# Kernel tuning notes

Measured on AMD Instinct MI355X. Metric: run time of the kernel, lower is better.

The kernel has to match this reference:

```python
import jax, jax.numpy as jnp
import numpy as np

N_NODES = 50000

def _gcn_layer(x, src, dst, W, b, n_nodes):
    # x: [N, F_in]; src/dst: [E+N] (self-loops already appended)
    h = x @ W  # [N, F_out]
    deg = jax.ops.segment_sum(jnp.ones_like(dst, dtype=h.dtype), dst, num_segments=n_nodes)
    dinv = jnp.where(deg > 0, jax.lax.rsqrt(deg), 0.0)  # deg^{-1/2}
    norm = dinv[src] * dinv[dst]  # [E+N]
    msg = h[src] * norm[:, None]  # gather + scale
    out = jax.ops.segment_sum(msg, dst, num_segments=n_nodes)  # scatter-add
    return out + b

def setup_inputs() -> dict:
    key = jax.random.key(0)
    k1, k2, k3, k4 = jax.random.split(key, 4)
    d = 128
    E = 800000
    x = jax.random.normal(k1, (N_NODES, d), dtype=jnp.float32)
    edge_index = jax.random.randint(k2, (2, E), 0, N_NODES, dtype=jnp.int64)
    W1 = jax.random.normal(k3, (d, d), dtype=jnp.float32) / np.sqrt(d)
    b1 = jnp.zeros((d,), dtype=jnp.float32)
    W2 = jax.random.normal(k4, (d, d), dtype=jnp.float32) / np.sqrt(d)
    b2 = jnp.zeros((d,), dtype=jnp.float32)
    return {"x": x, "edge_index": edge_index, "W1": W1, "b1": b1, "W2": W2, "b2": b2}

def reference(x, edge_index, W1, b1, W2, b2):
    n = x.shape[0]
    loops = jnp.arange(n, dtype=edge_index.dtype)
    src = jnp.concatenate([edge_index[0], loops])  # add self-loops
    dst = jnp.concatenate([edge_index[1], loops])
    h = _gcn_layer(x, src, dst, W1, b1, n)
    h = jax.nn.relu(h)
    z = _gcn_layer(h, src, dst, W2, b2, n)
    return z
```

## Files before the change

### kernel.cpp

```cpp
#include <hip/hip_runtime.h>
#include <hip/hip_fp16.h>

#define NF 128
#define DMAX 64

typedef _Float16 half8  __attribute__((ext_vector_type(8)));
typedef _Float16 half4v __attribute__((ext_vector_type(4)));
typedef float    floatx4 __attribute__((ext_vector_type(4)));

__global__ __launch_bounds__(256) void z_k(
    int* __restrict__ cnt, int N, int zb,
    const float* __restrict__ W1, const float* __restrict__ W2,
    __half* __restrict__ WT1, __half* __restrict__ WT2)
{
    int b = blockIdx.x;
    if (b < zb) {
        int i = b * 256 + threadIdx.x;
        if (i <= N) cnt[i] = 0;
        return;
    }
    int idx = (b - zb) * 256 + threadIdx.x;
    const float* W = (idx < 16384) ? W1 : W2;
    __half* WT     = (idx < 16384) ? WT1 : WT2;
    int j = idx & 16383;
    int nn = j & 127, k = j >> 7;
    WT[nn * NF + k] = __float2half(W[k * NF + nn]);
}

__device__ __forceinline__ void fill_one(
    int d, int s, int* __restrict__ cnt, int* __restrict__ csrF,
    int* __restrict__ ovf, int N)
{
    int pos = atomicAdd(&cnt[d], 1);
    if (pos < DMAX) {
        csrF[(size_t)d * DMAX + pos] = s;
    } else {
        int o = atomicAdd(&cnt[N], 1);
        ovf[2 * o] = d; ovf[2 * o + 1] = s;
    }
}

__global__ __launch_bounds__(256) void fill_k(
    const int* __restrict__ src, const int* __restrict__ dst,
    int* __restrict__ cnt, int* __restrict__ csrF, int* __restrict__ ovf,
    int E, int N)
{
    int i4 = (blockIdx.x * 256 + threadIdx.x) * 4;
    if (i4 + 3 < E) {
        int4 d = *(const int4*)(dst + i4);
        int4 s = *(const int4*)(src + i4);
        fill_one(d.x, s.x, cnt, csrF, ovf, N);
        fill_one(d.y, s.y, cnt, csrF, ovf, N);
        fill_one(d.z, s.z, cnt, csrF, ovf, N);
        fill_one(d.w, s.w, cnt, csrF, ovf, N);
    } else {
        for (int e = i4; e < E; e++)
            fill_one(dst[e], src[e], cnt, csrF, ovf, N);
    }
}

__global__ __launch_bounds__(512) void gemm1_k(
    const float* __restrict__ X, const __half* __restrict__ WT,
    const int* __restrict__ cnt, __half* __restrict__ H, int M)
{
    __shared__ __half wlds[128][136];
    const int tid = threadIdx.x;
    {
        int r = tid >> 2;
        int c0 = (tid & 3) * 32;
        const half8* s = (const half8*)(WT + (size_t)r * NF + c0);
        half8* d = (half8*)&wlds[r][c0];
        #pragma unroll
        for (int j = 0; j < 4; j++) d[j] = s[j];
    }
    __syncthreads();

    const int wave = tid >> 6, lane = tid & 63;
    const int quad = lane >> 4, l15 = lane & 15;
    const int rowA = blockIdx.x * 128 + wave * 16 + l15;
    const int rowc = (rowA < M) ? rowA : (M - 1);

    half8 afr[4];
    #pragma unroll
    for (int kc = 0; kc < 4; kc++) {
        const floatx4* p = (const floatx4*)(X + (size_t)rowc * NF + kc * 32 + quad * 8);
        floatx4 u = p[0], v = p[1];
        half8 a;
        a[0] = (_Float16)u[0]; a[1] = (_Float16)u[1];
        a[2] = (_Float16)u[2]; a[3] = (_Float16)u[3];
        a[4] = (_Float16)v[0]; a[5] = (_Float16)v[1];
        a[6] = (_Float16)v[2]; a[7] = (_Float16)v[3];
        afr[kc] = a;
    }

    floatx4 acc[8];
    #pragma unroll
    for (int ct = 0; ct < 8; ct++) { floatx4 z = {0.f, 0.f, 0.f, 0.f}; acc[ct] = z; }

    #pragma unroll
    for (int kc = 0; kc < 4; kc++) {
        #pragma unroll
        for (int ct = 0; ct < 8; ct++) {
            half8 b = *(const half8*)&wlds[ct * 16 + l15][kc * 32 + quad * 8];
            acc[ct] = __builtin_amdgcn_mfma_f32_16x16x32_f16(afr[kc], b, acc[ct], 0, 0, 0);
        }
    }

    const int orow0 = blockIdx.x * 128 + wave * 16 + quad * 4;
    #pragma unroll
    for (int r = 0; r < 4; r++) {
        int orow = orow0 + r;
        if (orow < M) {
            float dv = rsqrtf((float)cnt[orow] + 1.0f);
            #pragma unroll
            for (int ct = 0; ct < 8; ct++)
                H[(size_t)orow * NF + ct * 16 + l15] = __float2half(acc[ct][r] * dv);
        }
    }
}

__device__ __forceinline__ void gather2w(
    const half8* __restrict__ hs8, const int* __restrict__ csrF,
    const int* __restrict__ cnt, int nA, int n,
    int g, int fl, int lane, floatx4& ac0, floatx4& ac1,
    const int* __restrict__ ovf, int novf)
{
    const int ep  = g & 1;
    const int isB = g >> 1;
    const int nB  = nA + 1;

    int cntA = (nA < n) ? cnt[nA] : 0;
    int cntB = (nB < n) ? cnt[nB] : 0;
    const int ccA = min(cntA, DMAX), ccB = min(cntB, DMAX);

    int idxA = (lane < ccA) ? __builtin_nontemporal_load(&csrF[(size_t)nA * DMAX + lane]) : 0;
    int idxB = (lane < ccB) ? __builtin_nontemporal_load(&csrF[(size_t)nB * DMAX + lane]) : 0;

    if (ep == 0) {
        int nd = isB ? nB : nA;
        if (nd < n) {
            half8 s = hs8[(size_t)nd * 16 + fl];
            ac0[0] += (float)s[0]; ac0[1] += (float)s[1];
            ac0[2] += (float)s[2]; ac0[3] += (float)s[3];
            ac1[0] += (float)s[4]; ac1[1] += (float)s[5];
            ac1[2] += (float)s[6]; ac1[3] += (float)s[7];
        }
    }

    const int myc  = isB ? ccB : ccA;
    const int maxc = max(ccA, ccB);
    for (int j = 0; j < maxc; j += 16) {
        int s[8];
        half8 v[8];
        #pragma unroll
        for (int t = 0; t < 8; t++) {
            int e = j + 2 * t + ep;
            int eA = min(e, ccA - 1); eA = (eA < 0) ? 0 : eA;
            int eB = min(e, ccB - 1); eB = (eB < 0) ? 0 : eB;
            int sa = __shfl(idxA, eA, 64);
            int sb = __shfl(idxB, eB, 64);
            s[t] = isB ? sb : sa;
        }
        #pragma unroll
        for (int t = 0; t < 8; t++)
            v[t] = hs8[(size_t)s[t] * 16 + fl];
        #pragma unroll
        for (int t = 0; t < 8; t++) {
            if (j + 2 * t + ep < myc) {
                ac0[0] += (float)v[t][0]; ac0[1] += (float)v[t][1];
                ac0[2] += (float)v[t][2]; ac0[3] += (float)v[t][3];
                ac1[0] += (float)v[t][4]; ac1[1] += (float)v[t][5];
                ac1[2] += (float)v[t][6]; ac1[3] += (float)v[t][7];
            }
        }
    }

    if (novf > 0 && ep == 0) {
        int myN = isB ? nB : nA;
        for (int i = 0; i < novf; i++) {
            int d = ovf[2 * i];
            if (d == myN) {
                half8 v = hs8[(size_t)ovf[2 * i + 1] * 16 + fl];
                ac0[0] += (float)v[0]; ac0[1] += (float)v[1];
                ac0[2] += (float)v[2]; ac0[3] += (float)v[3];
                ac1[0] += (float)v[4]; ac1[1] += (float)v[5];
                ac1[2] += (float)v[6]; ac1[3] += (float)v[7];
            }
        }
    }

    #pragma unroll
    for (int q = 0; q < 4; q++) {
        ac0[q] += __shfl_xor(ac0[q], 16, 64);
        ac1[q] += __shfl_xor(ac1[q], 16, 64);
    }
}

__global__ __launch_bounds__(512) void aggmm_k(
    const __half* __restrict__ hs, const int* __restrict__ csrF,
    const int* __restrict__ cnt, const float* __restrict__ bias,
    const __half* __restrict__ WT, __half* __restrict__ Hout, int n,
    const int* __restrict__ ovf)
{
    __shared__ __half alds[16][136];
    const int tid = threadIdx.x;
    const int wave = tid >> 6, lane = tid & 63;
    const int g = lane >> 4, fl = lane & 15;
    const int nb0 = blockIdx.x * 16;
    const int nA = nb0 + wave * 2;
    const int novf = cnt[n];

    floatx4 ac0 = {0.f, 0.f, 0.f, 0.f}, ac1 = {0.f, 0.f, 0.f, 0.f};
    gather2w((const half8*)hs, csrF, cnt, nA, n, g, fl, lane, ac0, ac1, ovf, novf);

    if ((g & 1) == 0) {
        int node = nA + (g >> 1);
        int row  = wave * 2 + (g >> 1);
        half8 hv;
        if (node < n) {
            float dv = rsqrtf((float)cnt[node] + 1.0f);
            const floatx4 bv0 = *(const floatx4*)&bias[fl * 8];
            const floatx4 bv1 = *(const floatx4*)&bias[fl * 8 + 4];
            hv[0] = (_Float16)fmaxf(dv * ac0[0] + bv0[0], 0.f);
            hv[1] = (_Float16)fmaxf(dv * ac0[1] + bv0[1], 0.f);
            hv[2] = (_Float16)fmaxf(dv * ac0[2] + bv0[2], 0.f);
            hv[3] = (_Float16)fmaxf(dv * ac0[3] + bv0[3], 0.f);
            hv[4] = (_Float16)fmaxf(dv * ac1[0] + bv1[0], 0.f);
            hv[5] = (_Float16)fmaxf(dv * ac1[1] + bv1[1], 0.f);
            hv[6] = (_Float16)fmaxf(dv * ac1[2] + bv1[2], 0.f);
            hv[7] = (_Float16)fmaxf(dv * ac1[3] + bv1[3], 0.f);
        } else {
            #pragma unroll
            for (int i = 0; i < 8; i++) hv[i] = (_Float16)0.f;
        }
        *(half8*)&alds[row][fl * 8] = hv;
    }
    __syncthreads();

    const int quad = lane >> 4, l15 = lane & 15;
    const int ct = wave;
    half8 afr[4];
    #pragma unroll
    for (int kc = 0; kc < 4; kc++)
        afr[kc] = *(const half8*)&alds[l15][kc * 32 + quad * 8];

    floatx4 o0 = {0.f, 0.f, 0.f, 0.f};
    #pragma unroll
    for (int kc = 0; kc < 4; kc++) {
        half8 b = *(const half8*)(WT + (size_t)(ct * 16 + l15) * NF + kc * 32 + quad * 8);
        o0 = __builtin_amdgcn_mfma_f32_16x16x32_f16(afr[kc], b, o0, 0, 0, 0);
    }

    #pragma unroll
    for (int r = 0; r < 4; r++) {
        int node = nb0 + quad * 4 + r;
        if (node < n) {
            float dv = rsqrtf((float)cnt[node] + 1.0f);
            Hout[(size_t)node * NF + ct * 16 + l15] = __float2half(o0[r] * dv);
        }
    }
}

__global__ __launch_bounds__(256) void agg4_k(
    const __half* __restrict__ hs, const int* __restrict__ csrF,
    const int* __restrict__ cnt, const float* __restrict__ bias,
    float* __restrict__ outf, int n, const int* __restrict__ ovf)
{
    const int tid = threadIdx.x;
    const int wave = tid >> 6, lane = tid & 63;
    const int g = lane >> 4, fl = lane & 15;
    const int nA = blockIdx.x * 8 + wave * 2;
    if (nA >= n) return;
    const int novf = cnt[n];

    floatx4 ac0 = {0.f, 0.f, 0.f, 0.f}, ac1 = {0.f, 0.f, 0.f, 0.f};
    gather2w((const half8*)hs, csrF, cnt, nA, n, g, fl, lane, ac0, ac1, ovf, novf);

    if ((g & 1) == 0) {
        int node = nA + (g >> 1);
        if (node < n) {
            float dv = rsqrtf((float)cnt[node] + 1.0f);
            const floatx4 bv0 = *(const floatx4*)&bias[fl * 8];
            const floatx4 bv1 = *(const floatx4*)&bias[fl * 8 + 4];
            floatx4 w0, w1;
            w0[0] = dv * ac0[0] + bv0[0]; w0[1] = dv * ac0[1] + bv0[1];
            w0[2] = dv * ac0[2] + bv0[2]; w0[3] = dv * ac0[3] + bv0[3];
            w1[0] = dv * ac1[0] + bv1[0]; w1[1] = dv * ac1[1] + bv1[1];
            w1[2] = dv * ac1[2] + bv1[2]; w1[3] = dv * ac1[3] + bv1[3];
            *(floatx4*)(outf + (size_t)node * NF + fl * 8)     = w0;
            *(floatx4*)(outf + (size_t)node * NF + fl * 8 + 4) = w1;
        }
    }
}


extern "C" void kernel_launch(void* const* d_in, const int* in_sizes, int n_in,
                              void* d_out, int out_size, void* d_ws, size_t ws_size,
                              hipStream_t stream) {
    const float* x  = (const float*)d_in[0];
    const int*   ei = (const int*)d_in[1];
    const float* W1 = (const float*)d_in[2];
    const float* b1 = (const float*)d_in[3];
    const float* W2 = (const float*)d_in[4];
    const float* b2 = (const float*)d_in[5];
    float* out = (float*)d_out;

    const int N = in_sizes[0] / NF;
    const int E = in_sizes[1] / 2;
    const int* src = ei;
    const int* dst = ei + E;

    char* ws = (char*)d_ws;
    size_t off = 0;
    auto alloc = [&](size_t bytes) {
        void* p = ws + off;
        off += bytes;
        off = (off + 63) & ~(size_t)63;
        return p;
    };
    int*    cnt  = (int*)alloc((size_t)(N + 1) * 4);
    int*    csrF = (int*)alloc((size_t)N * DMAX * 4);
    int*    ovf  = (int*)alloc((size_t)E * 2 * 4);
    __half* WT1  = (__half*)alloc((size_t)NF * NF * 2);
    __half* WT2  = (__half*)alloc((size_t)NF * NF * 2);
    __half* H16  = (__half*)alloc((size_t)N * NF * 2);
    __half* A16  = (__half*)alloc((size_t)N * NF * 2);

    int zb = (N + 1 + 255) / 256;
    int fbF = (E + 1023) / 1024;
    int GB  = (N + 127) / 128;
    int mb  = (N + 15) / 16;
    int ab  = (N + 7) / 8;

    z_k<<<zb + 128, 256, 0, stream>>>(cnt, N, zb, W1, W2, WT1, WT2);
    fill_k<<<fbF, 256, 0, stream>>>(src, dst, cnt, csrF, ovf, E, N);
    gemm1_k<<<GB, 512, 0, stream>>>(x, WT1, cnt, H16, N);
    aggmm_k<<<mb, 512, 0, stream>>>(H16, csrF, cnt, b1, WT2, A16, N, ovf);
    agg4_k<<<ab, 256, 0, stream>>>(A16, csrF, cnt, b2, out, N, ovf);
}
```

Baseline: 210.8 us.

## Co-schedule edge fill and first GEMM in one kernel, defer degree scaling

```diff
diff --git a/kernel.cpp b/kernel.cpp
--- a/kernel.cpp
+++ b/kernel.cpp
@@ -27,43 +27,10 @@
     WT[nn * NF + k] = __float2half(W[k * NF + nn]);
 }
 
-__device__ __forceinline__ void fill_one(
-    int d, int s, int* __restrict__ cnt, int* __restrict__ csrF,
-    int* __restrict__ ovf, int N)
-{
-    int pos = atomicAdd(&cnt[d], 1);
-    if (pos < DMAX) {
-        csrF[(size_t)d * DMAX + pos] = s;
-    } else {
-        int o = atomicAdd(&cnt[N], 1);
-        ovf[2 * o] = d; ovf[2 * o + 1] = s;
-    }
-}
-
-__global__ __launch_bounds__(256) void fill_k(
-    const int* __restrict__ src, const int* __restrict__ dst,
-    int* __restrict__ cnt, int* __restrict__ csrF, int* __restrict__ ovf,
-    int E, int N)
-{
-    int i4 = (blockIdx.x * 256 + threadIdx.x) * 4;
-    if (i4 + 3 < E) {
-        int4 d = *(const int4*)(dst + i4);
-        int4 s = *(const int4*)(src + i4);
-        fill_one(d.x, s.x, cnt, csrF, ovf, N);
-        fill_one(d.y, s.y, cnt, csrF, ovf, N);
-        fill_one(d.z, s.z, cnt, csrF, ovf, N);
-        fill_one(d.w, s.w, cnt, csrF, ovf, N);
-    } else {
-        for (int e = i4; e < E; e++)
-            fill_one(dst[e], src[e], cnt, csrF, ovf, N);
-    }
-}
-
-__global__ __launch_bounds__(512) void gemm1_k(
+__device__ __forceinline__ void gemm1raw_body(
     const float* __restrict__ X, const __half* __restrict__ WT,
-    const int* __restrict__ cnt, __half* __restrict__ H, int M)
-{
-    __shared__ __half wlds[128][136];
+    float* __restrict__ H32, int M, int bid, __half (*wlds)[136])
+{
     const int tid = threadIdx.x;
     {
         int r = tid >> 2;
@@ -77,7 +44,7 @@
 
     const int wave = tid >> 6, lane = tid & 63;
     const int quad = lane >> 4, l15 = lane & 15;
-    const int rowA = blockIdx.x * 128 + wave * 16 + l15;
+    const int rowA = bid * 128 + wave * 16 + l15;
     const int rowc = (rowA < M) ? rowA : (M - 1);
 
     half8 afr[4];
@@ -106,17 +73,62 @@
         }
     }
 
-    const int orow0 = blockIdx.x * 128 + wave * 16 + quad * 4;
+    const int orow0 = bid * 128 + wave * 16 + quad * 4;
     #pragma unroll
     for (int r = 0; r < 4; r++) {
         int orow = orow0 + r;
         if (orow < M) {
-            float dv = rsqrtf((float)cnt[orow] + 1.0f);
             #pragma unroll
             for (int ct = 0; ct < 8; ct++)
-                H[(size_t)orow * NF + ct * 16 + l15] = __float2half(acc[ct][r] * dv);
-        }
-    }
+                H32[(size_t)orow * NF + ct * 16 + l15] = acc[ct][r];
+        }
+    }
+}
+
+__global__ __launch_bounds__(512) void mix_k(
+    const int* __restrict__ src, const int* __restrict__ dst,
+    int* __restrict__ cnt, int* __restrict__ csrF, int* __restrict__ ovf,
+    int E, int N,
+    const float* __restrict__ X, const __half* __restrict__ WT,
+    float* __restrict__ H32, int GB)
+{
+    __shared__ __half wlds[128][136];
+    const int b = blockIdx.x;
+    const bool isGemm = ((b % 5) == 0) && (b / 5 < GB);
+    if (isGemm) {
+        gemm1raw_body(X, WT, H32, N, b / 5, wlds);
+        return;
+    }
+    const int fid = (b < 5 * GB) ? (b - (b / 5 + 1)) : (b - GB);
+    int e = fid * 512 + (int)threadIdx.x;
+    if (e < E) {
+        int d = dst[e], s = src[e];
+        int pos = atomicAdd(&cnt[d], 1);
+        if (pos < DMAX) {
+            csrF[(size_t)d * DMAX + pos] = s;
+        } else {
+            int o = atomicAdd(&cnt[N], 1);
+            ovf[2 * o] = d; ovf[2 * o + 1] = s;
+        }
+    }
+}
+
+__global__ __launch_bounds__(256) void scale_k(
+    const float* __restrict__ H32, const int* __restrict__ cnt,
+    __half* __restrict__ H16, int n)
+{
+    int i = blockIdx.x * 256 + threadIdx.x;
+    int row = i >> 4, j = i & 15;
+    if (row >= n) return;
+    float dv = rsqrtf((float)cnt[row] + 1.0f);
+    const floatx4* p = (const floatx4*)(H32 + (size_t)row * NF + j * 8);
+    floatx4 u = p[0], v = p[1];
+    half8 h;
+    h[0] = (_Float16)(u[0] * dv); h[1] = (_Float16)(u[1] * dv);
+    h[2] = (_Float16)(u[2] * dv); h[3] = (_Float16)(u[3] * dv);
+    h[4] = (_Float16)(v[0] * dv); h[5] = (_Float16)(v[1] * dv);
+    h[6] = (_Float16)(v[2] * dv); h[7] = (_Float16)(v[3] * dv);
+    *(half8*)&H16[(size_t)row * NF + j * 8] = h;
 }
 
 __device__ __forceinline__ void gather2w(
@@ -321,20 +333,23 @@
     int*    cnt  = (int*)alloc((size_t)(N + 1) * 4);
     int*    csrF = (int*)alloc((size_t)N * DMAX * 4);
     int*    ovf  = (int*)alloc((size_t)E * 2 * 4);
+    float*  H32  = (float*)alloc((size_t)N * NF * 4);
     __half* WT1  = (__half*)alloc((size_t)NF * NF * 2);
     __half* WT2  = (__half*)alloc((size_t)NF * NF * 2);
     __half* H16  = (__half*)alloc((size_t)N * NF * 2);
     __half* A16  = (__half*)alloc((size_t)N * NF * 2);
 
-    int zb = (N + 1 + 255) / 256;
-    int fbF = (E + 1023) / 1024;
+    int zb  = (N + 1 + 255) / 256;
     int GB  = (N + 127) / 128;
+    int fb  = (E + 511) / 512;
+    int sb  = (N * 16 + 255) / 256;
     int mb  = (N + 15) / 16;
     int ab  = (N + 7) / 8;
 
     z_k<<<zb + 128, 256, 0, stream>>>(cnt, N, zb, W1, W2, WT1, WT2);
-    fill_k<<<fbF, 256, 0, stream>>>(src, dst, cnt, csrF, ovf, E, N);
-    gemm1_k<<<GB, 512, 0, stream>>>(x, WT1, cnt, H16, N);
+    mix_k<<<fb + GB, 512, 0, stream>>>(src, dst, cnt, csrF, ovf, E, N,
+                                       x, WT1, H32, GB);
+    scale_k<<<sb, 256, 0, stream>>>(H32, cnt, H16, N);
     aggmm_k<<<mb, 512, 0, stream>>>(H16, csrF, cnt, b1, WT2, A16, N, ovf);
     agg4_k<<<ab, 256, 0, stream>>>(A16, csrF, cnt, b2, out, N, ovf);
 }
```

Measured after the change: 209.7 us. No clear change (-0.5%).
